# Optimization experiments

Measured on AMD Instinct MI355X. Metric: run time of the kernel, lower is better.

The kernel has to match this reference:

```python
import jax, jax.numpy as jnp
import numpy as np

T, B, H, I = 128, 32, 256, 256


def setup_inputs() -> dict:
    key = jax.random.key(0)
    ks = jax.random.split(key, 8)
    s = 0.05
    embs = jax.random.normal(ks[0], (T, B, I), jnp.float32)
    lens = jax.random.randint(ks[1], (B,), 1, T + 1)  # lengths in [1, T]
    W_ih = jax.random.normal(ks[2], (4 * H, I), jnp.float32) * s
    W_hh = jax.random.normal(ks[3], (4 * H, H), jnp.float32) * s
    b_ih = jax.random.normal(ks[4], (4 * H,), jnp.float32) * s
    b_hh = jax.random.normal(ks[5], (4 * H,), jnp.float32) * s
    W_a = jax.random.normal(ks[6], (H, 2 * H), jnp.float32) * s  # attention combine (Luong-style)
    b_a = jax.random.normal(ks[7], (H,), jnp.float32) * s
    return {"embs": embs, "lens": lens, "W_ih": W_ih, "W_hh": W_hh,
            "b_ih": b_ih, "b_hh": b_hh, "W_a": W_a, "b_a": b_a}


def reference(embs, lens, W_ih, W_hh, b_ih, b_hh, W_a, b_a):
    Tn, Bn, _ = embs.shape
    Hn = W_hh.shape[1]
    t_idx = jnp.arange(Tn)

    def step(carry, inp):
        h, c, buf, h_fin, c_fin = carry  # h,c: [B,H]; buf: [T,B,H] history of outputs
        t, emb = inp
        # dot-product attention of current hidden over past outputs (steps < t)
        scores = jnp.einsum('tbh,bh->tb', buf, h)
        valid = (t_idx < t)[:, None]
        alpha = jax.nn.softmax(jnp.where(valid, scores, -1e9), axis=0)
        ctx = jnp.einsum('tb,tbh->bh', alpha, buf)
        h_att = jnp.tanh(jnp.concatenate([ctx, h], axis=-1) @ W_a.T + b_a)
        h = jnp.where(t > 0, h_att, h)  # no history at t=0
        # standard PyTorch LSTM cell (gate order i,f,g,o)
        gates = emb @ W_ih.T + b_ih + h @ W_hh.T + b_hh
        i_g, f_g, g_g, o_g = jnp.split(gates, 4, axis=-1)
        c = jax.nn.sigmoid(f_g) * c + jax.nn.sigmoid(i_g) * jnp.tanh(g_g)
        h = jax.nn.sigmoid(o_g) * jnp.tanh(c)
        buf = buf.at[t].set(h)
        take = (t == lens - 1)[:, None]
        h_fin = jnp.where(take, h, h_fin)
        c_fin = jnp.where(take, c, c_fin)
        return (h, c, buf, h_fin, c_fin), h

    z = jnp.zeros((Bn, Hn), embs.dtype)
    buf0 = jnp.zeros((Tn, Bn, Hn), embs.dtype)
    carry, output = jax.lax.scan(step, (z, z, buf0, z, z), (t_idx, embs))
    # output: [T,B,H]; final (h,c) gathered at t == lens-1: [B,H]
    return output, carry[3], carry[4]
```

## Files before the change

### kernel.cpp

```cpp
#include <hip/hip_runtime.h>


#define T_DIM 128
#define B_DIM 32

typedef _Float16 half2_t __attribute__((ext_vector_type(2)));

static __device__ __forceinline__ unsigned pack2(float a, float b) {
  half2_t h;
  h.x = (_Float16)a;
  h.y = (_Float16)b;
  return __builtin_bit_cast(unsigned, h);
}

static __device__ __forceinline__ float dot2f(unsigned w, unsigned v, float acc) {
  half2_t a = __builtin_bit_cast(half2_t, w);
  half2_t b = __builtin_bit_cast(half2_t, v);
#if __has_builtin(__builtin_amdgcn_fdot2)
  return __builtin_amdgcn_fdot2(a, b, acc, false);
#else
  return acc + (float)a.x * (float)b.x + (float)a.y * (float)b.y;
#endif
}

static __device__ __forceinline__ float dot8(uint4 w, uint4 v, float acc) {
  acc = dot2f(w.x, v.x, acc);
  acc = dot2f(w.y, v.y, acc);
  acc = dot2f(w.z, v.z, acc);
  acc = dot2f(w.w, v.w, acc);
  return acc;
}

static __device__ __forceinline__ float lo16(unsigned u) {
  return (float)__builtin_bit_cast(half2_t, u).x;
}
static __device__ __forceinline__ float hi16(unsigned u) {
  return (float)__builtin_bit_cast(half2_t, u).y;
}

static __device__ __forceinline__ float fsig(float x) {
  return __builtin_amdgcn_rcpf(1.f + __expf(-x));
}
static __device__ __forceinline__ float ftanh(float x) {
  float e = __expf(2.f * x);
  return 1.f - 2.f * __builtin_amdgcn_rcpf(e + 1.f);
}

__global__ void pack_weights(const float* __restrict__ W_ih, const float* __restrict__ W_hh,
                             const float* __restrict__ W_a, unsigned* __restrict__ Wih16,
                             uint4* __restrict__ Whh_pack, uint4* __restrict__ Wa_pack,
                             unsigned long long* __restrict__ ywp,
                             unsigned long long* __restrict__ psx) {
  int n = blockIdx.x * 256 + threadIdx.x;
  if (n < 131072) {
    int k2 = n >> 10, r = n & 1023;
    const float* src = W_ih + r * 256 + 2 * k2;
    Wih16[n] = pack2(src[0], src[1]);
  }
  if (n < 32768) {
    int m = n >> 12, tid = (n >> 3) & 511, i = n & 7;
    int r_local = tid >> 2, qk = tid & 3;
    int q = r_local >> 5, jl = r_local & 31;
    int r = q * 256 + m * 32 + jl;
    const float* src = W_hh + r * 256 + (4 * i + qk) * 8;
    uint4 v;
    v.x = pack2(src[0], src[1]);
    v.y = pack2(src[2], src[3]);
    v.z = pack2(src[4], src[5]);
    v.w = pack2(src[6], src[7]);
    Whh_pack[n] = v;
  }
  if (n < 16384) {
    int m = n >> 11, j = (n >> 3) & 255, c = n & 7;
    int col0 = (c < 4) ? (m * 32 + c * 8) : (256 + m * 32 + (c - 4) * 8);
    const float* src = W_a + j * 512 + col0;
    uint4 v;
    v.x = pack2(src[0], src[1]);
    v.y = pack2(src[2], src[3]);
    v.z = pack2(src[4], src[5]);
    v.w = pack2(src[6], src[7]);
    Wa_pack[n] = v;
  }
  if (n < 65536)
    __hip_atomic_store(&ywp[n], 0ull, __ATOMIC_RELAXED, __HIP_MEMORY_SCOPE_AGENT);
  else if (n < 81920)
    __hip_atomic_store(&psx[n - 65536], 0ull, __ATOMIC_RELAXED, __HIP_MEMORY_SCOPE_AGENT);
}

__global__ void compute_gih(const float* __restrict__ embs, const unsigned* __restrict__ Wih16,
                            const float* __restrict__ b_ih, const float* __restrict__ b_hh,
                            float* __restrict__ gih) {
  __shared__ unsigned embS16[16][128];
  const int tid = threadIdx.x;
  const int tb0 = blockIdx.x * 16;
  for (int x = tid; x < 2048; x += 256) {
    int e = x >> 7, p = x & 127;
    const float* s = embs + (size_t)(tb0 + e) * 256 + 2 * p;
    embS16[e][p] = pack2(s[0], s[1]);
  }
  __syncthreads();
  float acc[16][4];
#pragma unroll
  for (int e = 0; e < 16; ++e)
#pragma unroll
    for (int q = 0; q < 4; ++q) acc[e][q] = 0.f;
  for (int k2 = 0; k2 < 128; ++k2) {
    unsigned w0 = Wih16[k2 * 1024 + tid];
    unsigned w1 = Wih16[k2 * 1024 + tid + 256];
    unsigned w2 = Wih16[k2 * 1024 + tid + 512];
    unsigned w3 = Wih16[k2 * 1024 + tid + 768];
#pragma unroll
    for (int e = 0; e < 16; ++e) {
      unsigned x = embS16[e][k2];
      acc[e][0] = dot2f(w0, x, acc[e][0]);
      acc[e][1] = dot2f(w1, x, acc[e][1]);
      acc[e][2] = dot2f(w2, x, acc[e][2]);
      acc[e][3] = dot2f(w3, x, acc[e][3]);
    }
  }
#pragma unroll
  for (int q = 0; q < 4; ++q) {
    float bias = b_ih[q * 256 + tid] + b_hh[q * 256 + tid];
#pragma unroll
    for (int e = 0; e < 16; ++e)
      gih[(size_t)(tb0 + e) * 1024 + q * 256 + tid] = acc[e][q] + bias;
  }
}

__global__ void __launch_bounds__(512, 1)
alstm_rec(const int* __restrict__ lens, const float* __restrict__ gih,
          const uint4* __restrict__ Whh_pack, const uint4* __restrict__ Wa_pack,
          const float* __restrict__ b_a, unsigned long long* __restrict__ ywp,
          unsigned long long* __restrict__ psx, float* __restrict__ out,
          float* __restrict__ hfin, float* __restrict__ cfin) {
  const int tid = threadIdx.x;
  const int b = blockIdx.x & 31;
  const int m = blockIdx.x >> 5;

  __shared__ __align__(16) unsigned histSl[128 * 20];
  __shared__ __align__(16) float ystoreF[128 * 256];
  __shared__ __align__(16) unsigned hp2[128];
  __shared__ __align__(16) unsigned hsl2[16];
  __shared__ float sc[128];
  __shared__ float zp[4][256];
  __shared__ float gsl[128];

  uint4 wh4[8];
  {
    const uint4* p = Whh_pack + ((size_t)m * 512 + tid) * 8;
#pragma unroll
    for (int i = 0; i < 8; ++i) wh4[i] = p[i];
  }
  uint4 way[4], waw[4];
  {
    const int j_pub = (tid - 128) & 255;
    const uint4* p = Wa_pack + ((size_t)m * 256 + j_pub) * 8;
#pragma unroll
    for (int i = 0; i < 4; ++i) way[i] = p[i];
#pragma unroll
    for (int i = 0; i < 4; ++i) waw[i] = p[4 + i];
  }
  const float ba_j = (tid < 256) ? b_a[tid] : 0.f;
  const int len_b = lens[b];
  const int r_local = tid >> 2, qk = tid & 3;
  const int gq = r_local >> 5, gjl = r_local & 31;

  if (tid < 128) hp2[tid] = 0u;
  float c_reg = 0.f;
  __syncthreads();

  for (int t = 0; t < T_DIM; ++t) {
    float gih_v = gih[((size_t)t * 32 + b) * 1024 + gq * 256 + m * 32 + gjl];
    float w_j = 0.f;

    if (t > 0) {
      if (tid < 256) {
        const unsigned long long* base = ywp + b * 2048 + tid;
        unsigned long long v[8];
        for (;;) {
          bool ok = true;
#pragma unroll
          for (int mm = 0; mm < 8; ++mm)
            v[mm] = __hip_atomic_load(base + mm * 256, __ATOMIC_RELAXED, __HIP_MEMORY_SCOPE_AGENT);
#pragma unroll
          for (int mm = 0; mm < 8; ++mm) ok &= ((unsigned)v[mm] == (unsigned)t);
          if (ok) break;
          __builtin_amdgcn_s_sleep(1);
        }
        float y = 0.f, w = 0.f;
#pragma unroll
        for (int mm = 0; mm < 8; ++mm) {
          unsigned pl = (unsigned)(v[mm] >> 32);
          y += lo16(pl);
          w += hi16(pl);
        }
        w_j = w;
        ystoreF[(t - 1) * 256 + tid] = y;
      } else if (tid >= 448) {
        const int lane = tid - 448;
        const unsigned long long* base = psx + b * 512 + lane;
        unsigned long long v[8];
        for (;;) {
          bool ok = true;
#pragma unroll
          for (int mm = 0; mm < 8; ++mm)
            v[mm] = __hip_atomic_load(base + mm * 64, __ATOMIC_RELAXED, __HIP_MEMORY_SCOPE_AGENT);
#pragma unroll
          for (int mm = 0; mm < 8; ++mm) ok &= ((unsigned)v[mm] == (unsigned)t);
          if (ok) break;
          __builtin_amdgcn_s_sleep(1);
        }
        float s0 = 0.f, s1 = 0.f;
#pragma unroll
        for (int mm = 0; mm < 8; ++mm) {
          unsigned pl = (unsigned)(v[mm] >> 32);
          s0 += lo16(pl);
          s1 += hi16(pl);
        }
        float v0 = (2 * lane < t) ? s0 : -3.0e38f;
        float v1 = (2 * lane + 1 < t) ? s1 : -3.0e38f;
        float mx = fmaxf(v0, v1);
#pragma unroll
        for (int off = 32; off >= 1; off >>= 1) mx = fmaxf(mx, __shfl_xor(mx, off));
        float e0 = (2 * lane < t) ? __expf(v0 - mx) : 0.f;
        float e1 = (2 * lane + 1 < t) ? __expf(v1 - mx) : 0.f;
        float sm = e0 + e1;
#pragma unroll
        for (int off = 32; off >= 1; off >>= 1) sm += __shfl_xor(sm, off);
        float inv = __builtin_amdgcn_rcpf(sm);
        sc[2 * lane] = e0 * inv;
        sc[2 * lane + 1] = e1 * inv;
      }
      __syncthreads();
      {
        const int sp = tid >> 7, p2 = tid & 127;
        float c0 = 0.f, c1 = 0.f;
        const float* yb = ystoreF + 2 * p2;
        for (int s = sp; s < t; s += 4) {
          float al = sc[s];
          float2 yv = *(const float2*)(yb + s * 256);
          c0 += al * yv.x;
          c1 += al * yv.y;
        }
        zp[sp][2 * p2] = c0;
        zp[sp][2 * p2 + 1] = c1;
      }
      __syncthreads();
      if (tid < 256) {
        float z = zp[0][tid] + zp[1][tid] + zp[2][tid] + zp[3][tid];
        float hv = ftanh(ba_j + w_j + z);
        float o = __shfl_xor(hv, 1);
        if (!(tid & 1)) hp2[tid >> 1] = pack2(hv, o);
      }
      __syncthreads();
    }
    {
      float a = 0.f;
#pragma unroll
      for (int i = 0; i < 8; ++i) {
        const int c = 4 * i + qk;
        uint4 hv = *(const uint4*)&hp2[c << 2];
        a = dot8(wh4[i], hv, a);
      }
      a += __shfl_xor(a, 1);
      a += __shfl_xor(a, 2);
      if (qk == 0) gsl[r_local] = a + gih_v;
    }
    __syncthreads();
    if (tid < 64) {
      if (tid < 32) {
        float ig = fsig(gsl[tid]);
        float fg = fsig(gsl[32 + tid]);
        float gg = ftanh(gsl[64 + tid]);
        float og = fsig(gsl[96 + tid]);
        float cn = fg * c_reg + ig * gg;
        float hn = og * ftanh(cn);
        c_reg = cn;
        out[((size_t)t * 32 + b) * 256 + m * 32 + tid] = hn;
        if (t == len_b - 1) {
          hfin[b * 256 + m * 32 + tid] = hn;
          cfin[b * 256 + m * 32 + tid] = cn;
        }
        float o = __shfl_xor(hn, 1);
        if (!(tid & 1)) {
          unsigned u = pack2(hn, o);
          hsl2[tid >> 1] = u;
          histSl[t * 20 + (tid >> 1)] = u;
        }
      }
      uint4 q0 = *(const uint4*)&hsl2[0];
      uint4 q1 = *(const uint4*)&hsl2[4];
      uint4 q2 = *(const uint4*)&hsl2[8];
      uint4 q3 = *(const uint4*)&hsl2[12];
      const int r0 = 2 * tid, r1 = 2 * tid + 1;
      float a0 = 0.f, a1 = 0.f;
      {
        uint4 h0, h1;
        h0 = *(const uint4*)&histSl[r0 * 20 + 0];
        h1 = *(const uint4*)&histSl[r1 * 20 + 0];
        a0 = dot8(h0, q0, a0);
        a1 = dot8(h1, q0, a1);
        h0 = *(const uint4*)&histSl[r0 * 20 + 4];
        h1 = *(const uint4*)&histSl[r1 * 20 + 4];
        a0 = dot8(h0, q1, a0);
        a1 = dot8(h1, q1, a1);
        h0 = *(const uint4*)&histSl[r0 * 20 + 8];
        h1 = *(const uint4*)&histSl[r1 * 20 + 8];
        a0 = dot8(h0, q2, a0);
        a1 = dot8(h1, q2, a1);
        h0 = *(const uint4*)&histSl[r0 * 20 + 12];
        h1 = *(const uint4*)&histSl[r1 * 20 + 12];
        a0 = dot8(h0, q3, a0);
        a1 = dot8(h1, q3, a1);
      }
      unsigned long long v = ((unsigned long long)pack2(a0, a1) << 32) |
                             (unsigned long long)(unsigned)(t + 1);
      __hip_atomic_store(&psx[b * 512 + m * 64 + tid], v, __ATOMIC_RELAXED,
                         __HIP_MEMORY_SCOPE_AGENT);
    }
    __syncthreads();
    if (tid >= 128 && tid < 384) {
      const int j = tid - 128;
      float ay = 0.f, aw = 0.f;
#pragma unroll
      for (int c = 0; c < 4; ++c) {
        uint4 hv = *(const uint4*)&hsl2[c * 4];
        ay = dot8(way[c], hv, ay);
        aw = dot8(waw[c], hv, aw);
      }
      unsigned long long v = ((unsigned long long)pack2(ay, aw) << 32) |
                             (unsigned long long)(unsigned)(t + 1);
      __hip_atomic_store(&ywp[b * 2048 + m * 256 + j], v, __ATOMIC_RELAXED,
                         __HIP_MEMORY_SCOPE_AGENT);
    }
  }
}

extern "C" void kernel_launch(void* const* d_in, const int* in_sizes, int n_in,
                              void* d_out, int out_size, void* d_ws, size_t ws_size,
                              hipStream_t stream) {
  const float* embs = (const float*)d_in[0];
  const int* lens = (const int*)d_in[1];
  const float* W_ih = (const float*)d_in[2];
  const float* W_hh = (const float*)d_in[3];
  const float* b_ih = (const float*)d_in[4];
  const float* b_hh = (const float*)d_in[5];
  const float* W_a = (const float*)d_in[6];
  const float* b_a = (const float*)d_in[7];

  float* out = (float*)d_out;
  float* hfin = out + (size_t)T_DIM * B_DIM * 256;
  float* cfin = hfin + (size_t)B_DIM * 256;

  char* ws = (char*)d_ws;
  float* gih = (float*)ws;
  unsigned* Wih16 = (unsigned*)(ws + 16777216);
  uint4* Whh_pack = (uint4*)(ws + 17301504);
  uint4* Wa_pack = (uint4*)(ws + 17825792);
  unsigned long long* ywp = (unsigned long long*)(ws + 18087936);
  unsigned long long* psx = (unsigned long long*)(ws + 18612224);

  pack_weights<<<1024, 256, 0, stream>>>(W_ih, W_hh, W_a, Wih16, Whh_pack, Wa_pack, ywp, psx);
  compute_gih<<<256, 256, 0, stream>>>(embs, Wih16, b_ih, b_hh, gih);
  alstm_rec<<<256, 512, 0, stream>>>(lens, gih, Whh_pack, Wa_pack, b_a, ywp, psx, out, hfin,
                                     cfin);
}
```

Baseline: 564.8 us.

## Restructure attention step: per-wave redundant LSTM cell, fp16 transposed history, max-free softmax

Each wave now recomputes the LSTM cell update redundantly, so the score and projection products can start without an extra block barrier. The c state is double-buffered in shared memory. The attention context is computed with one thread per output column doing packed fp16 dot products over a transposed fp16 history. This replaces the split-reduction pass and the two syncthreads around it. The softmax drops the max-subtraction reduction and clamps the exponent instead, and polling now waits per word rather than reloading all eight. The trade-off is reduced precision (fp16 context weights) and a risk of overflow-related inaccuracy if scores are large.

```diff
diff --git a/kernel.cpp b/kernel.cpp
--- a/kernel.cpp
+++ b/kernel.cpp
@@ -44,6 +44,15 @@
 static __device__ __forceinline__ float ftanh(float x) {
   float e = __expf(2.f * x);
   return 1.f - 2.f * __builtin_amdgcn_rcpf(e + 1.f);
+}
+
+static __device__ __forceinline__ unsigned long long wait_word(
+    const unsigned long long* p, unsigned want, unsigned long long v) {
+  while ((unsigned)v != want) {
+    __builtin_amdgcn_s_sleep(1);
+    v = __hip_atomic_load(p, __ATOMIC_RELAXED, __HIP_MEMORY_SCOPE_AGENT);
+  }
+  return v;
 }
 
 __global__ void pack_weights(const float* __restrict__ W_ih, const float* __restrict__ W_hh,
@@ -136,14 +145,15 @@
   const int tid = threadIdx.x;
   const int b = blockIdx.x & 31;
   const int m = blockIdx.x >> 5;
-
+  const int wv = tid >> 6, lane = tid & 63;
+
+  __shared__ __align__(16) unsigned yT[256 * 82];
   __shared__ __align__(16) unsigned histSl[128 * 20];
-  __shared__ __align__(16) float ystoreF[128 * 256];
   __shared__ __align__(16) unsigned hp2[128];
-  __shared__ __align__(16) unsigned hsl2[16];
-  __shared__ float sc[128];
-  __shared__ float zp[4][256];
+  __shared__ __align__(16) unsigned hslw[8 * 16];
+  __shared__ __align__(16) unsigned scA[64];
   __shared__ float gsl[128];
+  __shared__ float c_sd[2][32];
 
   uint4 wh4[8];
   {
@@ -165,11 +175,13 @@
   const int r_local = tid >> 2, qk = tid & 3;
   const int gq = r_local >> 5, gjl = r_local & 31;
 
+  for (int x = tid; x < 256 * 82; x += 512) yT[x] = 0u;
   if (tid < 128) hp2[tid] = 0u;
-  float c_reg = 0.f;
+  if (tid < 32) c_sd[0][tid] = 0.f;
   __syncthreads();
 
   for (int t = 0; t < T_DIM; ++t) {
+    const int par = t & 1;
     float gih_v = gih[((size_t)t * 32 + b) * 1024 + gq * 256 + m * 32 + gjl];
     float w_j = 0.f;
 
@@ -177,16 +189,11 @@
       if (tid < 256) {
         const unsigned long long* base = ywp + b * 2048 + tid;
         unsigned long long v[8];
-        for (;;) {
-          bool ok = true;
-#pragma unroll
-          for (int mm = 0; mm < 8; ++mm)
-            v[mm] = __hip_atomic_load(base + mm * 256, __ATOMIC_RELAXED, __HIP_MEMORY_SCOPE_AGENT);
-#pragma unroll
-          for (int mm = 0; mm < 8; ++mm) ok &= ((unsigned)v[mm] == (unsigned)t);
-          if (ok) break;
-          __builtin_amdgcn_s_sleep(1);
-        }
+#pragma unroll
+        for (int mm = 0; mm < 8; ++mm)
+          v[mm] = __hip_atomic_load(base + mm * 256, __ATOMIC_RELAXED, __HIP_MEMORY_SCOPE_AGENT);
+#pragma unroll
+        for (int mm = 0; mm < 8; ++mm) v[mm] = wait_word(base + mm * 256, (unsigned)t, v[mm]);
         float y = 0.f, w = 0.f;
 #pragma unroll
         for (int mm = 0; mm < 8; ++mm) {
@@ -195,21 +202,15 @@
           w += hi16(pl);
         }
         w_j = w;
-        ystoreF[(t - 1) * 256 + tid] = y;
-      } else if (tid >= 448) {
-        const int lane = tid - 448;
+        ((_Float16*)yT)[tid * 164 + (t - 1)] = (_Float16)y;
+      } else if (wv == 7) {
         const unsigned long long* base = psx + b * 512 + lane;
         unsigned long long v[8];
-        for (;;) {
-          bool ok = true;
-#pragma unroll
-          for (int mm = 0; mm < 8; ++mm)
-            v[mm] = __hip_atomic_load(base + mm * 64, __ATOMIC_RELAXED, __HIP_MEMORY_SCOPE_AGENT);
-#pragma unroll
-          for (int mm = 0; mm < 8; ++mm) ok &= ((unsigned)v[mm] == (unsigned)t);
-          if (ok) break;
-          __builtin_amdgcn_s_sleep(1);
-        }
+#pragma unroll
+        for (int mm = 0; mm < 8; ++mm)
+          v[mm] = __hip_atomic_load(base + mm * 64, __ATOMIC_RELAXED, __HIP_MEMORY_SCOPE_AGENT);
+#pragma unroll
+        for (int mm = 0; mm < 8; ++mm) v[mm] = wait_word(base + mm * 64, (unsigned)t, v[mm]);
         float s0 = 0.f, s1 = 0.f;
 #pragma unroll
         for (int mm = 0; mm < 8; ++mm) {
@@ -217,37 +218,25 @@
           s0 += lo16(pl);
           s1 += hi16(pl);
         }
-        float v0 = (2 * lane < t) ? s0 : -3.0e38f;
-        float v1 = (2 * lane + 1 < t) ? s1 : -3.0e38f;
-        float mx = fmaxf(v0, v1);
-#pragma unroll
-        for (int off = 32; off >= 1; off >>= 1) mx = fmaxf(mx, __shfl_xor(mx, off));
-        float e0 = (2 * lane < t) ? __expf(v0 - mx) : 0.f;
-        float e1 = (2 * lane + 1 < t) ? __expf(v1 - mx) : 0.f;
+        float e0 = (2 * lane < t) ? __expf(fminf(s0, 60.f)) : 0.f;
+        float e1 = (2 * lane + 1 < t) ? __expf(fminf(s1, 60.f)) : 0.f;
         float sm = e0 + e1;
 #pragma unroll
         for (int off = 32; off >= 1; off >>= 1) sm += __shfl_xor(sm, off);
         float inv = __builtin_amdgcn_rcpf(sm);
-        sc[2 * lane] = e0 * inv;
-        sc[2 * lane + 1] = e1 * inv;
-      }
-      __syncthreads();
-      {
-        const int sp = tid >> 7, p2 = tid & 127;
-        float c0 = 0.f, c1 = 0.f;
-        const float* yb = ystoreF + 2 * p2;
-        for (int s = sp; s < t; s += 4) {
-          float al = sc[s];
-          float2 yv = *(const float2*)(yb + s * 256);
-          c0 += al * yv.x;
-          c1 += al * yv.y;
-        }
-        zp[sp][2 * p2] = c0;
-        zp[sp][2 * p2 + 1] = c1;
+        scA[lane] = pack2(e0 * inv, e1 * inv);
       }
       __syncthreads();
       if (tid < 256) {
-        float z = zp[0][tid] + zp[1][tid] + zp[2][tid] + zp[3][tid];
+        float z = 0.f;
+        const unsigned* yrow = yT + tid * 82;
+        const int imax = (t + 3) >> 2;
+        for (int i = 0; i < imax; ++i) {
+          uint2 yv = *(const uint2*)(yrow + 2 * i);
+          uint2 av = *(const uint2*)(scA + 2 * i);
+          z = dot2f(yv.x, av.x, z);
+          z = dot2f(yv.y, av.y, z);
+        }
         float hv = ftanh(ba_j + w_j + z);
         float o = __shfl_xor(hv, 1);
         if (!(tid & 1)) hp2[tid >> 1] = pack2(hv, o);
@@ -267,34 +256,36 @@
       if (qk == 0) gsl[r_local] = a + gih_v;
     }
     __syncthreads();
-    if (tid < 64) {
-      if (tid < 32) {
-        float ig = fsig(gsl[tid]);
-        float fg = fsig(gsl[32 + tid]);
-        float gg = ftanh(gsl[64 + tid]);
-        float og = fsig(gsl[96 + tid]);
-        float cn = fg * c_reg + ig * gg;
-        float hn = og * ftanh(cn);
-        c_reg = cn;
-        out[((size_t)t * 32 + b) * 256 + m * 32 + tid] = hn;
-        if (t == len_b - 1) {
-          hfin[b * 256 + m * 32 + tid] = hn;
-          cfin[b * 256 + m * 32 + tid] = cn;
+    {
+      const int e = lane & 31;
+      float g0 = gsl[e], g1 = gsl[32 + e], g2 = gsl[64 + e], g3 = gsl[96 + e];
+      float cold = c_sd[par][e];
+      float ig = fsig(g0);
+      float fg = fsig(g1);
+      float gg = ftanh(g2);
+      float og = fsig(g3);
+      float cn = fg * cold + ig * gg;
+      float hn = og * ftanh(cn);
+      float o = __shfl_xor(hn, 1);
+      if (lane < 32 && !(lane & 1)) hslw[wv * 16 + (lane >> 1)] = pack2(hn, o);
+      uint4 q0 = *(const uint4*)&hslw[wv * 16 + 0];
+      uint4 q1 = *(const uint4*)&hslw[wv * 16 + 4];
+      uint4 q2 = *(const uint4*)&hslw[wv * 16 + 8];
+      uint4 q3 = *(const uint4*)&hslw[wv * 16 + 12];
+
+      if (wv == 0) {
+        if (lane < 32) {
+          out[((size_t)t * 32 + b) * 256 + m * 32 + lane] = hn;
+          c_sd[par ^ 1][lane] = cn;
+          if (t == len_b - 1) {
+            hfin[b * 256 + m * 32 + lane] = hn;
+            cfin[b * 256 + m * 32 + lane] = cn;
+          }
         }
-        float o = __shfl_xor(hn, 1);
-        if (!(tid & 1)) {
-          unsigned u = pack2(hn, o);
-          hsl2[tid >> 1] = u;
-          histSl[t * 20 + (tid >> 1)] = u;
-        }
-      }
-      uint4 q0 = *(const uint4*)&hsl2[0];
-      uint4 q1 = *(const uint4*)&hsl2[4];
-      uint4 q2 = *(const uint4*)&hsl2[8];
-      uint4 q3 = *(const uint4*)&hsl2[12];
-      const int r0 = 2 * tid, r1 = 2 * tid + 1;
-      float a0 = 0.f, a1 = 0.f;
-      {
+      } else if (wv == 1) {
+        if (lane < 32 && !(lane & 1)) histSl[t * 20 + (lane >> 1)] = pack2(hn, o);
+        const int r0 = 2 * lane, r1 = 2 * lane + 1;
+        float a0 = 0.f, a1 = 0.f;
         uint4 h0, h1;
         h0 = *(const uint4*)&histSl[r0 * 20 + 0];
         h1 = *(const uint4*)&histSl[r1 * 20 + 0];
@@ -312,26 +303,26 @@
         h1 = *(const uint4*)&histSl[r1 * 20 + 12];
         a0 = dot8(h0, q3, a0);
         a1 = dot8(h1, q3, a1);
+        unsigned long long v = ((unsigned long long)pack2(a0, a1) << 32) |
+                               (unsigned long long)(unsigned)(t + 1);
+        __hip_atomic_store(&psx[b * 512 + m * 64 + lane], v, __ATOMIC_RELAXED,
+                           __HIP_MEMORY_SCOPE_AGENT);
+      } else if (wv >= 2 && wv <= 5) {
+        const int j = tid - 128;
+        float ay = 0.f, aw = 0.f;
+        ay = dot8(way[0], q0, ay);
+        aw = dot8(waw[0], q0, aw);
+        ay = dot8(way[1], q1, ay);
+        aw = dot8(waw[1], q1, aw);
+        ay = dot8(way[2], q2, ay);
+        aw = dot8(waw[2], q2, aw);
+        ay = dot8(way[3], q3, ay);
+        aw = dot8(waw[3], q3, aw);
+        unsigned long long v = ((unsigned long long)pack2(ay, aw) << 32) |
+                               (unsigned long long)(unsigned)(t + 1);
+        __hip_atomic_store(&ywp[b * 2048 + m * 256 + j], v, __ATOMIC_RELAXED,
+                           __HIP_MEMORY_SCOPE_AGENT);
       }
-      unsigned long long v = ((unsigned long long)pack2(a0, a1) << 32) |
-                             (unsigned long long)(unsigned)(t + 1);
-      __hip_atomic_store(&psx[b * 512 + m * 64 + tid], v, __ATOMIC_RELAXED,
-                         __HIP_MEMORY_SCOPE_AGENT);
-    }
-    __syncthreads();
-    if (tid >= 128 && tid < 384) {
-      const int j = tid - 128;
-      float ay = 0.f, aw = 0.f;
-#pragma unroll
-      for (int c = 0; c < 4; ++c) {
-        uint4 hv = *(const uint4*)&hsl2[c * 4];
-        ay = dot8(way[c], hv, ay);
-        aw = dot8(waw[c], hv, aw);
-      }
-      unsigned long long v = ((unsigned long long)pack2(ay, aw) << 32) |
-                             (unsigned long long)(unsigned)(t + 1);
-      __hip_atomic_store(&ywp[b * 2048 + m * 256 + j], v, __ATOMIC_RELAXED,
-                         __HIP_MEMORY_SCOPE_AGENT);
     }
   }
 }
```

After: 650.7 us. 1.15x slower.
